# Kernel optimization log

Measured on AMD Instinct MI355X. Metric: run time of the kernel, lower is better.

## Reference

```python
import jax, jax.numpy as jnp
import numpy as np


def setup_inputs() -> dict:
    key0 = jax.random.key(0)
    kq, kk, kv = jax.random.split(key0, 3)
    B, S, H, KVH, D = 1, 4096, 8, 2, 64
    return {
        "query": jax.random.normal(kq, (B, S, H, D), dtype=jnp.float32),
        "key": jax.random.normal(kk, (B, S, KVH, D), dtype=jnp.float32),
        "value": jax.random.normal(kv, (B, S, KVH, D), dtype=jnp.float32),
    }


def _ring_attn_single(query, key, value):
    # world_size == 1 (dist uninitialized): ring loop is a single local step
    # with query_offset == key_offset == 0.
    B, S, H, D = query.shape
    KVH = key.shape[2]
    scale = D ** -0.5
    # [B, H, S, D]
    q = query.transpose(0, 2, 1, 3)
    k = key.transpose(0, 2, 1, 3)
    v = value.transpose(0, 2, 1, 3)
    if KVH != H:
        rep = H // KVH
        k = jnp.repeat(k, rep, axis=1)  # repeat_interleave on head dim
        v = jnp.repeat(v, rep, axis=1)
    logits = jnp.einsum("bhqd,bhkd->bhqk", q, k) * scale
    pos = jnp.arange(S)
    causal = pos[:, None] < pos[None, :]  # mask future keys
    logits = jnp.where(causal[None, None], -jnp.inf, logits)
    w = jax.nn.softmax(logits, axis=-1)  # [B, H, S, S]
    attn_out = jnp.einsum("bhqk,bhkd->bhqd", w, v)
    cw = jnp.sum(w, axis=-1, keepdims=True)  # chunk softmax mass (== 1)
    out = attn_out * cw / (cw + 1e-8)  # weight-accumulation renorm
    return out.transpose(0, 2, 1, 3)  # [B, S, H, D]


def reference(query, key, value):
    return _ring_attn_single(query, key, value)
```

## Files before the change

kernel.cpp:

```cpp
#include <hip/hip_runtime.h>
#include <hip/hip_bf16.h>


#define S_LEN 4096
#define H_Q   8
#define H_KV  2
#define DH    64
#define BN    64
#define NEG_BIG (-1e30f)
#define CS (0.125f * 1.44269504088896340736f)

#define CHUNK 8
#define NTR   144
#define KB_SH (S_LEN * H_KV * DH)
#define TILE_SH 4096
#define KVH_SH  (S_LEN * DH)
#define OB_SH    ((size_t)NTR * H_Q * 128 * DH)
#define L_FLOATS ((size_t)NTR * H_Q * 128)
#define WS_NEED ((size_t)(2 * KB_SH) * 2 + OB_SH * 2 + L_FLOATS * 4)

typedef __attribute__((ext_vector_type(8))) short bf16x8;
typedef __attribute__((ext_vector_type(4))) short s16x4;
typedef __attribute__((ext_vector_type(4))) float f32x4;
typedef __attribute__((ext_vector_type(4))) unsigned int u32x4;

__device__ __forceinline__ short bf(float x) {
    return __builtin_bit_cast(short, __float2bfloat16(x));
}
__device__ __forceinline__ float fbf(short u) {
    return __builtin_bit_cast(float, ((unsigned int)(unsigned short)u) << 16);
}
__device__ __forceinline__ unsigned int cvtpk(float lo, float hi) {
    unsigned int r;
    asm("v_cvt_pk_bf16_f32 %0, %1, %2" : "=v"(r) : "v"(lo), "v"(hi));
    return r;
}
__device__ __forceinline__ void gload16(const short* gp, short* lp) {
    __builtin_amdgcn_global_load_lds(
        (const __attribute__((address_space(1))) unsigned int*)gp,
        (__attribute__((address_space(3))) unsigned int*)lp, 16, 0, 0);
}

__global__ __launch_bounds__(256)
void ring_attn_prepass(const float* __restrict__ K, const float* __restrict__ V,
                       short* __restrict__ Kb, short* __restrict__ Vt) {
    const int b = blockIdx.x;
    const int t = threadIdx.x;
    if (b < 512) {
        const int i = (b * 256 + t) * 4;
        const int s   = i >> 7;
        const int kvh = (i >> 6) & 1;
        const int d   = i & 63;
        float4 kv = *(const float4*)(K + i);
        const int dst = kvh * KVH_SH + (s >> 6) * TILE_SH + (s & 63) * 64
                      + (((d >> 3) ^ (s & 7)) * 8) + (d & 7);
        *(unsigned int*)(Kb + dst)     = cvtpk(kv.x, kv.y);
        *(unsigned int*)(Kb + dst + 2) = cvtpk(kv.z, kv.w);
    } else {
        __shared__ short T[DH * 72];
        const int bb  = b - 512;
        const int kvh = bb >> 6;
        const int j   = bb & 63;
        const int s0  = j * 64;
        {
            const int r  = t >> 2;
            const int dq = (t & 3) * 16;
            const float* vp = V + ((s0 + r) * H_KV + kvh) * DH + dq;
            float4 a0 = *(const float4*)(vp);
            float4 a1 = *(const float4*)(vp + 4);
            float4 a2 = *(const float4*)(vp + 8);
            float4 a3 = *(const float4*)(vp + 12);
            float e[16] = {a0.x,a0.y,a0.z,a0.w, a1.x,a1.y,a1.z,a1.w,
                           a2.x,a2.y,a2.z,a2.w, a3.x,a3.y,a3.z,a3.w};
#pragma unroll
            for (int i2 = 0; i2 < 16; ++i2)
                T[(dq + i2) * 72 + r] = bf(e[i2]);
        }
        __syncthreads();
        {
            const int d = t >> 2;
            const int q = t & 3;
            s16x4 g0 = *(const s16x4*)(&T[d * 72 + 4 * q]);
            s16x4 g1 = *(const s16x4*)(&T[d * 72 + 16 + 4 * q]);
            s16x4 g2 = *(const s16x4*)(&T[d * 72 + 32 + 4 * q]);
            s16x4 g3 = *(const s16x4*)(&T[d * 72 + 48 + 4 * q]);
            bf16x8 x0 = bf16x8{g0[0],g0[1],g0[2],g0[3], g1[0],g1[1],g1[2],g1[3]};
            bf16x8 x1 = bf16x8{g2[0],g2[1],g2[2],g2[3], g3[0],g3[1],g3[2],g3[3]};
            short* base = Vt + kvh * KVH_SH + j * TILE_SH + d * 64;
            *(bf16x8*)(base + ((2 * q)     ^ (d & 7)) * 8) = x0;
            *(bf16x8*)(base + ((2 * q + 1) ^ (d & 7)) * 8) = x1;
        }
    }
}

template <bool SPLIT>
__global__ __launch_bounds__(256, 4)
void ring_attn_fwd(const float* __restrict__ Q, const short* __restrict__ Kb,
                   const short* __restrict__ Vt, float* __restrict__ O,
                   short* __restrict__ Obuf, float* __restrict__ Lbuf) {
    const int bid = blockIdx.x;
    const int h   = bid & 7;
    int qt, nch, jbeg, jend, tr0;
    if (SPLIT) {
        const int tr = (NTR - 1) - (bid >> 3);
        int g = 0, base = 0;
        for (;;) {
            const int cnt2 = 4 * (g + 1);
            if (tr < base + cnt2) break;
            base += cnt2; ++g;
        }
        const int u  = tr - base;
        const int qq = u / (g + 1);
        const int ch = u - qq * (g + 1);
        qt   = 4 * g + qq;
        nch  = g + 1;
        tr0  = base + qq * (g + 1);
        jbeg = ch * CHUNK;
        jend = min(2 * qt + 2, jbeg + CHUNK);
    } else {
        qt = 31 - (bid >> 3);
        nch = 1; jbeg = 0; jend = 2 * qt + 2; tr0 = 0;
    }
    const int kvh = h >> 2;

    __shared__ short Ksb[2][4096];
    __shared__ short Vsb[2][4096];

    const int tid  = threadIdx.x;
    const int w    = tid >> 6;
    const int lane = tid & 63;
    const int c    = lane & 15;
    const int q    = lane >> 4;
    const int e    = c & 7;

    bf16x8 qf[2][2];
#pragma unroll
    for (int st = 0; st < 2; ++st) {
        const int qg = qt * 128 + st * 64 + w * 16 + c;
        const float* qp = Q + (qg * H_Q + h) * DH + q * 8;
        float4 a0 = *(const float4*)(qp);
        float4 a1 = *(const float4*)(qp + 4);
        float4 b0 = *(const float4*)(qp + 32);
        float4 b1 = *(const float4*)(qp + 36);
        u32x4 u0 = {cvtpk(a0.x*CS, a0.y*CS), cvtpk(a0.z*CS, a0.w*CS),
                    cvtpk(a1.x*CS, a1.y*CS), cvtpk(a1.z*CS, a1.w*CS)};
        u32x4 u1 = {cvtpk(b0.x*CS, b0.y*CS), cvtpk(b0.z*CS, b0.w*CS),
                    cvtpk(b1.x*CS, b1.y*CS), cvtpk(b1.z*CS, b1.w*CS)};
        qf[st][0] = __builtin_bit_cast(bf16x8, u0);
        qf[st][1] = __builtin_bit_cast(bf16x8, u1);
    }

    f32x4 acc[2][4] = {};
    float l_a[2] = {0.f, 0.f}, l_b[2] = {0.f, 0.f};

    const short* gkb = Kb + kvh * KVH_SH + w * 1024 + lane * 8;
    const short* gvb = Vt + kvh * KVH_SH + w * 1024 + lane * 8;
#define STAGE(buf, j)                                             \
    do {                                                          \
        const short* gk = gkb + (j) * TILE_SH;                    \
        const short* gv = gvb + (j) * TILE_SH;                    \
        short* lk = &Ksb[buf][w * 1024];                          \
        short* lv = &Vsb[buf][w * 1024];                          \
        gload16(gk, lk);        gload16(gk + 512, lk + 512);      \
        gload16(gv, lv);        gload16(gv + 512, lv + 512);      \
    } while (0)

    STAGE(0, jbeg);

    for (int j = jbeg; j < jend; ++j) {
        const int cur = (j - jbeg) & 1;
        __syncthreads();
        if (j + 1 < jend)
            STAGE(cur ^ 1, j + 1);

        const short* Kc = Ksb[cur];
        const short* Vc = Vsb[cur];

        f32x4 s[2][4] = {};
#pragma unroll
        for (int nt = 0; nt < 4; ++nt) {
            const int rb = (nt * 16 + c) * 64;
            bf16x8 kf0 = *(const bf16x8*)(Kc + rb + (q ^ e) * 8);
            bf16x8 kf1 = *(const bf16x8*)(Kc + rb + ((q + 4) ^ e) * 8);
            s[0][nt] = __builtin_amdgcn_mfma_f32_16x16x32_bf16(kf0, qf[0][0], s[0][nt], 0, 0, 0);
            s[0][nt] = __builtin_amdgcn_mfma_f32_16x16x32_bf16(kf1, qf[0][1], s[0][nt], 0, 0, 0);
            s[1][nt] = __builtin_amdgcn_mfma_f32_16x16x32_bf16(kf0, qf[1][0], s[1][nt], 0, 0, 0);
            s[1][nt] = __builtin_amdgcn_mfma_f32_16x16x32_bf16(kf1, qf[1][1], s[1][nt], 0, 0, 0);
        }

        bf16x8 pf[2][2];
#pragma unroll
        for (int st = 0; st < 2; ++st) {
            if (j >= 2 * qt + st) {
                const int koff = (j - 2 * qt - st) * 64;
                const int qrl  = w * 16 + c;
#pragma unroll
                for (int nt = 0; nt < 4; ++nt) {
                    const int kl = koff + nt * 16 + q * 4;
#pragma unroll
                    for (int r = 0; r < 4; ++r)
                        if (kl + r > qrl) s[st][nt][r] = NEG_BIG;
                }
            }
#pragma unroll
            for (int nt = 0; nt < 4; ++nt)
#pragma unroll
                for (int r = 0; r < 4; ++r) {
                    const float p = __builtin_amdgcn_exp2f(s[st][nt][r]);
                    s[st][nt][r] = p;
                    if (nt & 1) l_b[st] += p; else l_a[st] += p;
                }
            u32x4 w0 = {cvtpk(s[st][0][0], s[st][0][1]), cvtpk(s[st][0][2], s[st][0][3]),
                        cvtpk(s[st][1][0], s[st][1][1]), cvtpk(s[st][1][2], s[st][1][3])};
            u32x4 w1 = {cvtpk(s[st][2][0], s[st][2][1]), cvtpk(s[st][2][2], s[st][2][3]),
                        cvtpk(s[st][3][0], s[st][3][1]), cvtpk(s[st][3][2], s[st][3][3])};
            pf[st][0] = __builtin_bit_cast(bf16x8, w0);
            pf[st][1] = __builtin_bit_cast(bf16x8, w1);
        }

#pragma unroll
        for (int dt = 0; dt < 4; ++dt) {
            const int nb = (dt * 16 + c) * 64;
            bf16x8 vf0 = *(const bf16x8*)(Vc + nb + ((2 * q)     ^ e) * 8);
            bf16x8 vf1 = *(const bf16x8*)(Vc + nb + ((2 * q + 1) ^ e) * 8);
            acc[0][dt] = __builtin_amdgcn_mfma_f32_16x16x32_bf16(pf[0][0], vf0, acc[0][dt], 0, 0, 0);
            acc[0][dt] = __builtin_amdgcn_mfma_f32_16x16x32_bf16(pf[0][1], vf1, acc[0][dt], 0, 0, 0);
            acc[1][dt] = __builtin_amdgcn_mfma_f32_16x16x32_bf16(pf[1][0], vf0, acc[1][dt], 0, 0, 0);
            acc[1][dt] = __builtin_amdgcn_mfma_f32_16x16x32_bf16(pf[1][1], vf1, acc[1][dt], 0, 0, 0);
        }
    }

    float lr[2][4], l_lane[2];
#pragma unroll
    for (int st = 0; st < 2; ++st) {
        float t2 = l_a[st] + l_b[st];
        t2 += __shfl_xor(t2, 16);
        t2 += __shfl_xor(t2, 32);
        l_lane[st] = t2;
#pragma unroll
        for (int r = 0; r < 4; ++r)
            lr[st][r] = __shfl(t2, q * 4 + r);
    }

    if (!SPLIT || nch == 1) {
#pragma unroll
        for (int st = 0; st < 2; ++st)
#pragma unroll
            for (int r = 0; r < 4; ++r) {
                const float inv = 1.0f / lr[st][r];
                const int row = qt * 128 + st * 64 + w * 16 + q * 4 + r;
                float* op = O + (row * H_Q + h) * DH + c;
#pragma unroll
                for (int dt = 0; dt < 4; ++dt)
                    op[dt * 16] = acc[st][dt][r] * inv;
            }
    } else {
        const int slot = (tr0 + jbeg / CHUNK) * 8 + h;
        short* ob = Obuf + (size_t)slot * (128 * DH);
#pragma unroll
        for (int st = 0; st < 2; ++st) {
#pragma unroll
            for (int r = 0; r < 4; ++r) {
                const int rin = st * 64 + w * 16 + q * 4 + r;
#pragma unroll
                for (int dt = 0; dt < 4; ++dt)
                    ob[rin * DH + dt * 16 + c] = bf(acc[st][dt][r]);
            }
            if (lane < 16)
                Lbuf[slot * 128 + st * 64 + w * 16 + lane] = l_lane[st];
        }
    }
}

__global__ __launch_bounds__(256)
void ring_attn_combine(const short* __restrict__ Obuf, const float* __restrict__ Lbuf,
                       float* __restrict__ O) {
    const int gid  = blockIdx.x * 256 + threadIdx.x;
    const int d0   = (gid & 7) * 8;
    const int h    = (gid >> 3) & 7;
    const int srow = 512 + (gid >> 6);
    const int qt   = srow >> 7;
    const int rin  = srow & 127;
    const int g    = qt >> 2;
    const int base = 2 * g * (g + 1);
    const int nch  = g + 1;
    const int tr0  = base + (qt - 4 * g) * nch;

    float num[8] = {};
    float den = 0.0f;
    for (int ch = 0; ch < nch; ++ch) {
        const int slot = (tr0 + ch) * 8 + h;
        den += Lbuf[slot * 128 + rin];
        bf16x8 v = *(const bf16x8*)(Obuf + (size_t)slot * (128 * DH) + rin * DH + d0);
#pragma unroll
        for (int i = 0; i < 8; ++i)
            num[i] += fbf(v[i]);
    }
    const float inv = 1.0f / den;
    float* op = O + (srow * H_Q + h) * DH + d0;
    *(float4*)(op)     = float4{num[0]*inv, num[1]*inv, num[2]*inv, num[3]*inv};
    *(float4*)(op + 4) = float4{num[4]*inv, num[5]*inv, num[6]*inv, num[7]*inv};
}

extern "C" void kernel_launch(void* const* d_in, const int* in_sizes, int n_in,
                              void* d_out, int out_size, void* d_ws, size_t ws_size,
                              hipStream_t stream) {
    const float* Q = (const float*)d_in[0];
    const float* K = (const float*)d_in[1];
    const float* V = (const float*)d_in[2];
    float* O  = (float*)d_out;
    short* Kb = (short*)d_ws;
    short* Vt = Kb + KB_SH;
    short* Obuf = Vt + KB_SH;
    float* Lbuf = (float*)(Obuf + OB_SH);

    ring_attn_prepass<<<640, 256, 0, stream>>>(K, V, Kb, Vt);
    if (ws_size >= WS_NEED) {
        ring_attn_fwd<true><<<NTR * H_Q, 256, 0, stream>>>(Q, Kb, Vt, O, Obuf, Lbuf);
        ring_attn_combine<<<(S_LEN - 512) * H_Q * DH / 8 / 256, 256, 0, stream>>>(Obuf, Lbuf, O);
    } else {
        ring_attn_fwd<false><<<32 * H_Q, 256, 0, stream>>>(Q, Kb, Vt, O, Obuf, Lbuf);
    }
}
```

Baseline: 100.9 us.

## Halve KV split chunk size and drop LDS double buffering

The KV chunk per split work item shrinks from 8 to 4 tiles, so the fixed grouping of query tiles per chunk count changes and the grid grows from 144 to 272 work items per head. The combine kernel's indexing changes to match. LDS double buffering is removed, and each tile is now loaded and then synchronised twice per iteration. The aim is finer load balance and lower LDS use for higher occupancy, at the cost of losing overlap between loads and compute and adding more partial outputs to combine.

```diff
diff --git a/kernel.cpp b/kernel.cpp
--- a/kernel.cpp
+++ b/kernel.cpp
@@ -10,8 +10,8 @@
 #define NEG_BIG (-1e30f)
 #define CS (0.125f * 1.44269504088896340736f)
 
-#define CHUNK 8
-#define NTR   144
+#define CHUNK 4
+#define NTR   272
 #define KB_SH (S_LEN * H_KV * DH)
 #define TILE_SH 4096
 #define KVH_SH  (S_LEN * DH)
@@ -105,14 +105,14 @@
         const int tr = (NTR - 1) - (bid >> 3);
         int g = 0, base = 0;
         for (;;) {
-            const int cnt2 = 4 * (g + 1);
+            const int cnt2 = 2 * (g + 1);
             if (tr < base + cnt2) break;
             base += cnt2; ++g;
         }
         const int u  = tr - base;
         const int qq = u / (g + 1);
         const int ch = u - qq * (g + 1);
-        qt   = 4 * g + qq;
+        qt   = 2 * g + qq;
         nch  = g + 1;
         tr0  = base + qq * (g + 1);
         jbeg = ch * CHUNK;
@@ -123,8 +123,8 @@
     }
     const int kvh = h >> 2;
 
-    __shared__ short Ksb[2][4096];
-    __shared__ short Vsb[2][4096];
+    __shared__ short Ksb[4096];
+    __shared__ short Vsb[4096];
 
     const int tid  = threadIdx.x;
     const int w    = tid >> 6;
@@ -155,33 +155,24 @@
 
     const short* gkb = Kb + kvh * KVH_SH + w * 1024 + lane * 8;
     const short* gvb = Vt + kvh * KVH_SH + w * 1024 + lane * 8;
-#define STAGE(buf, j)                                             \
-    do {                                                          \
-        const short* gk = gkb + (j) * TILE_SH;                    \
-        const short* gv = gvb + (j) * TILE_SH;                    \
-        short* lk = &Ksb[buf][w * 1024];                          \
-        short* lv = &Vsb[buf][w * 1024];                          \
-        gload16(gk, lk);        gload16(gk + 512, lk + 512);      \
-        gload16(gv, lv);        gload16(gv + 512, lv + 512);      \
-    } while (0)
-
-    STAGE(0, jbeg);
 
     for (int j = jbeg; j < jend; ++j) {
-        const int cur = (j - jbeg) & 1;
+        {
+            const short* gk = gkb + j * TILE_SH;
+            const short* gv = gvb + j * TILE_SH;
+            short* lk = &Ksb[w * 1024];
+            short* lv = &Vsb[w * 1024];
+            gload16(gk, lk);        gload16(gk + 512, lk + 512);
+            gload16(gv, lv);        gload16(gv + 512, lv + 512);
+        }
         __syncthreads();
-        if (j + 1 < jend)
-            STAGE(cur ^ 1, j + 1);
-
-        const short* Kc = Ksb[cur];
-        const short* Vc = Vsb[cur];
 
         f32x4 s[2][4] = {};
 #pragma unroll
         for (int nt = 0; nt < 4; ++nt) {
             const int rb = (nt * 16 + c) * 64;
-            bf16x8 kf0 = *(const bf16x8*)(Kc + rb + (q ^ e) * 8);
-            bf16x8 kf1 = *(const bf16x8*)(Kc + rb + ((q + 4) ^ e) * 8);
+            bf16x8 kf0 = *(const bf16x8*)(Ksb + rb + (q ^ e) * 8);
+            bf16x8 kf1 = *(const bf16x8*)(Ksb + rb + ((q + 4) ^ e) * 8);
             s[0][nt] = __builtin_amdgcn_mfma_f32_16x16x32_bf16(kf0, qf[0][0], s[0][nt], 0, 0, 0);
             s[0][nt] = __builtin_amdgcn_mfma_f32_16x16x32_bf16(kf1, qf[0][1], s[0][nt], 0, 0, 0);
             s[1][nt] = __builtin_amdgcn_mfma_f32_16x16x32_bf16(kf0, qf[1][0], s[1][nt], 0, 0, 0);
@@ -221,13 +212,14 @@
 #pragma unroll
         for (int dt = 0; dt < 4; ++dt) {
             const int nb = (dt * 16 + c) * 64;
-            bf16x8 vf0 = *(const bf16x8*)(Vc + nb + ((2 * q)     ^ e) * 8);
-            bf16x8 vf1 = *(const bf16x8*)(Vc + nb + ((2 * q + 1) ^ e) * 8);
+            bf16x8 vf0 = *(const bf16x8*)(Vsb + nb + ((2 * q)     ^ e) * 8);
+            bf16x8 vf1 = *(const bf16x8*)(Vsb + nb + ((2 * q + 1) ^ e) * 8);
             acc[0][dt] = __builtin_amdgcn_mfma_f32_16x16x32_bf16(pf[0][0], vf0, acc[0][dt], 0, 0, 0);
             acc[0][dt] = __builtin_amdgcn_mfma_f32_16x16x32_bf16(pf[0][1], vf1, acc[0][dt], 0, 0, 0);
             acc[1][dt] = __builtin_amdgcn_mfma_f32_16x16x32_bf16(pf[1][0], vf0, acc[1][dt], 0, 0, 0);
             acc[1][dt] = __builtin_amdgcn_mfma_f32_16x16x32_bf16(pf[1][1], vf1, acc[1][dt], 0, 0, 0);
         }
+        __syncthreads();
     }
 
     float lr[2][4], l_lane[2];
@@ -278,13 +270,13 @@
     const int gid  = blockIdx.x * 256 + threadIdx.x;
     const int d0   = (gid & 7) * 8;
     const int h    = (gid >> 3) & 7;
-    const int srow = 512 + (gid >> 6);
+    const int srow = 256 + (gid >> 6);
     const int qt   = srow >> 7;
     const int rin  = srow & 127;
-    const int g    = qt >> 2;
-    const int base = 2 * g * (g + 1);
+    const int g    = qt >> 1;
+    const int base = g * (g + 1);
     const int nch  = g + 1;
-    const int tr0  = base + (qt - 4 * g) * nch;
+    const int tr0  = base + (qt & 1) * nch;
 
     float num[8] = {};
     float den = 0.0f;
@@ -317,7 +309,7 @@
     ring_attn_prepass<<<640, 256, 0, stream>>>(K, V, Kb, Vt);
     if (ws_size >= WS_NEED) {
         ring_attn_fwd<true><<<NTR * H_Q, 256, 0, stream>>>(Q, Kb, Vt, O, Obuf, Lbuf);
-        ring_attn_combine<<<(S_LEN - 512) * H_Q * DH / 8 / 256, 256, 0, stream>>>(Obuf, Lbuf, O);
+        ring_attn_combine<<<(S_LEN - 256) * H_Q * DH / 8 / 256, 256, 0, stream>>>(Obuf, Lbuf, O);
     } else {
         ring_attn_fwd<false><<<32 * H_Q, 256, 0, stream>>>(Q, Kb, Vt, O, Obuf, Lbuf);
     }
```

New measurement: 105.4 us. 1.04x slower.
